# Kernel tuning notes

Measured on AMD Instinct MI355X. Metric: run time of the kernel, lower is better.

## Reference

```python
import jax, jax.numpy as jnp
import numpy as np

B, T, DIM, H = 2, 2048, 1024, 16
HD = DIM // H


def setup_inputs() -> dict:
    key = jax.random.key(0)
    k1, k2, k3 = jax.random.split(key, 3)
    std = 1.0 / np.sqrt(DIM)
    x = jax.random.normal(k1, (B, T, DIM), dtype=jnp.float32)
    # torch Linear(dim, 3*dim).weight is [3*dim, dim]; we store the transposed
    # [dim, 3*dim] layout so forward is x @ W_qkv (same math).
    W_qkv = jax.random.uniform(k2, (DIM, 3 * DIM), dtype=jnp.float32, minval=-std, maxval=std)
    W_proj = jax.random.uniform(k3, (DIM, DIM), dtype=jnp.float32, minval=-std, maxval=std)
    return {"x": x, "W_qkv": W_qkv, "W_proj": W_proj}


def reference(x, W_qkv, W_proj):
    Bv, Tv, C = x.shape
    # qkv projection -> [B, T, 3, H, HD] -> q,k,v each [B, H, T, HD]
    qkv = (x @ W_qkv).reshape(Bv, Tv, 3, H, HD)
    qkv = jnp.transpose(qkv, (2, 0, 3, 1, 4))
    q, k, v = qkv[0], qkv[1], qkv[2]
    scale = jnp.asarray(np.sqrt(HD), dtype=x.dtype)
    scores = jnp.einsum('bhqd,bhkd->bhqk', q, k) / scale
    causal = jnp.tril(jnp.ones((Tv, Tv), dtype=bool))  # [T, T]
    scores = jnp.where(causal[None, None, :, :], scores, -jnp.inf)
    attn = jax.nn.softmax(scores, axis=-1)  # [B, H, T, T]
    # entropy per query position, averaged over heads -> [B, T]
    entropy = -(attn * jnp.log(attn + 1e-9)).sum(axis=-1).mean(axis=1)
    # dropout is identity in eval mode
    out = jnp.einsum('bhqk,bhkd->bhqd', attn, v)
    out = jnp.transpose(out, (0, 2, 1, 3)).reshape(Bv, Tv, C)
    return out @ W_proj, entropy
```

## Files before the change

kernel.cpp:

```cpp
#include <hip/hip_runtime.h>


typedef unsigned short u16;
typedef __attribute__((ext_vector_type(8))) __bf16 bf16x8;
typedef __attribute__((ext_vector_type(4))) float float4v;

#define BQ 2
#define TQ 2048
#define DIMQ 1024
#define HQ 16
#define HDQ 64

__device__ __forceinline__ float4v mfma16(bf16x8 a, bf16x8 b, float4v c) {
    return __builtin_amdgcn_mfma_f32_16x16x32_bf16(a, b, c, 0, 0, 0);
}

__device__ __forceinline__ u16 f2bf(float f) {
    unsigned x = __float_as_uint(f);
    return (u16)((x + 0x7FFFu + ((x >> 16) & 1u)) >> 16);
}

__device__ __forceinline__ uint4 cvt8(float4 a, float4 b) {
    union { uint4 v; u16 u[8]; } r;
    r.u[0] = f2bf(a.x); r.u[1] = f2bf(a.y); r.u[2] = f2bf(a.z); r.u[3] = f2bf(a.w);
    r.u[4] = f2bf(b.x); r.u[5] = f2bf(b.y); r.u[6] = f2bf(b.z); r.u[7] = f2bf(b.w);
    return r.v;
}

__device__ __forceinline__ void async16(const u16* g, u16* l) {
    __builtin_amdgcn_global_load_lds(
        (const __attribute__((address_space(1))) void*)g,
        (__attribute__((address_space(3))) void*)l, 16, 0, 0);
}

__device__ __forceinline__ void tr_tile(
    const float* __restrict__ in, u16* __restrict__ out, int R, int C,
    int tx, int ty, int tid, float (*T)[68])
{
    const int k0 = ty * 64, n0 = tx * 64;
    {
        int r = tid >> 2, cc = (tid & 3) << 4;
        const float* src = in + (size_t)(k0 + r) * C + n0 + cc;
        float4 v0 = ((const float4*)src)[0];
        float4 v1 = ((const float4*)src)[1];
        float4 v2 = ((const float4*)src)[2];
        float4 v3 = ((const float4*)src)[3];
        *(float4*)&T[r][cc + 0]  = v0;
        *(float4*)&T[r][cc + 4]  = v1;
        *(float4*)&T[r][cc + 8]  = v2;
        *(float4*)&T[r][cc + 12] = v3;
    }
    __syncthreads();
    {
        int nr = tid >> 2, kc = (tid & 3) << 4;
        union { uint4 v; u16 u[8]; } o0, o1;
#pragma unroll
        for (int j = 0; j < 8; ++j) o0.u[j] = f2bf(T[kc + j][nr]);
#pragma unroll
        for (int j = 0; j < 8; ++j) o1.u[j] = f2bf(T[kc + 8 + j][nr]);
        u16* dst = out + (size_t)(n0 + nr) * R + k0 + kc;
        ((uint4*)dst)[0] = o0.v;
        *(uint4*)(dst + 8) = o1.v;
    }
}

__global__ __launch_bounds__(256) void prep_kernel(
    const float* __restrict__ x, const float* __restrict__ Wq,
    const float* __restrict__ Wp,
    u16* __restrict__ xb, u16* __restrict__ Wt, u16* __restrict__ Wpt)
{
    __shared__ float T[64][68];
    const int bx = blockIdx.x, tid = threadIdx.x;
    if (bx < 2048) {
        int i = (bx * 256 + tid) * 8;
        float4 a = *(const float4*)(x + i);
        float4 b = *(const float4*)(x + i + 4);
        *(uint4*)(xb + i) = cvt8(a, b);
    } else if (bx < 2816) {
        int bb = bx - 2048;
        tr_tile(Wq, Wt, DIMQ, 3 * DIMQ, bb % 48, bb / 48, tid, T);
    } else {
        int bb = bx - 2816;
        tr_tile(Wp, Wpt, DIMQ, DIMQ, bb & 15, bb >> 4, tid, T);
    }
}

__global__ __launch_bounds__(256) void tr_cvt(
    const float* __restrict__ in, u16* __restrict__ out, int R, int C)
{
    __shared__ float T[64][68];
    tr_tile(in, out, R, C, blockIdx.x, blockIdx.y, threadIdx.x, T);
}

template <int TILEM, int MODE>
__global__ __launch_bounds__(256) void gemm_db(
    const u16* __restrict__ A, const u16* __restrict__ Bt,
    int M, int N, int K,
    u16* __restrict__ Qo, u16* __restrict__ Ko, u16* __restrict__ Vt,
    float* __restrict__ Of, const float* __restrict__ EntIn)
{
    constexpr int MT = TILEM / 32;
    constexpr int AR = TILEM / 64;
    __shared__ u16 As[2][TILEM * 32];
    __shared__ u16 Bs[2][128 * 32];

    const int tid = threadIdx.x;
    const int bm = blockIdx.y, bn = blockIdx.x;
    const int wave = tid >> 6, lane = tid & 63;
    const int quad = lane >> 4, c = lane & 15;
    const int wm = wave >> 1, wn = wave & 1;
    const int x3 = c & 3;

    const float4v z = {0.f, 0.f, 0.f, 0.f};
    float4v acc[MT][4];
#pragma unroll
    for (int mt = 0; mt < MT; ++mt)
#pragma unroll
        for (int tn = 0; tn < 4; ++tn) acc[mt][tn] = z;

    const int srow = tid >> 2;
    const int schunk8 = (((tid & 3) ^ (srow & 3)) << 3);
    const u16* ga = A  + (size_t)(bm * TILEM + srow) * K + schunk8;
    const u16* gb = Bt + (size_t)(bn * 128  + srow) * K + schunk8;

#pragma unroll
    for (int p = 0; p < AR; ++p)
        async16(ga + (size_t)(p * 64) * K, As[0] + p * 2048 + tid * 8);
#pragma unroll
    for (int p = 0; p < 2; ++p)
        async16(gb + (size_t)(p * 64) * K, Bs[0] + p * 2048 + tid * 8);

    const int niter = K >> 5;
    for (int it = 0; it < niter; ++it) {
        __syncthreads();
        if (it + 1 < niter) {
            const int nb = (it + 1) & 1;
            const int kc = (it + 1) * 32;
#pragma unroll
            for (int p = 0; p < AR; ++p)
                async16(ga + kc + (size_t)(p * 64) * K, As[nb] + p * 2048 + tid * 8);
#pragma unroll
            for (int p = 0; p < 2; ++p)
                async16(gb + kc + (size_t)(p * 64) * K, Bs[nb] + p * 2048 + tid * 8);
        }
        const u16* as = As[it & 1];
        const u16* bs = Bs[it & 1];

        bf16x8 af[MT], bfr[4];
#pragma unroll
        for (int mt = 0; mt < MT; ++mt)
            af[mt] = *(const bf16x8*)&as[(wm * (TILEM / 2) + mt * 16 + c) * 32 +
                                         ((quad ^ x3) << 3)];
#pragma unroll
        for (int tn = 0; tn < 4; ++tn)
            bfr[tn] = *(const bf16x8*)&bs[(wn * 64 + tn * 16 + c) * 32 +
                                          ((quad ^ x3) << 3)];
#pragma unroll
        for (int mt = 0; mt < MT; ++mt)
#pragma unroll
            for (int tn = 0; tn < 4; ++tn)
                acc[mt][tn] = mfma16(af[mt], bfr[tn], acc[mt][tn]);
    }

#pragma unroll
    for (int mt = 0; mt < MT; ++mt)
#pragma unroll
        for (int tn = 0; tn < 4; ++tn) {
            int gm0 = bm * TILEM + wm * (TILEM / 2) + mt * 16 + quad * 4;
            int gn  = bn * 128 + wn * 64 + tn * 16 + c;
            if (MODE == 0) {
                int s = gn >> 10, h = (gn >> 6) & 15, d = gn & 63;
                int b = gm0 >> 11, t0 = gm0 & 2047;
                size_t bh = (size_t)(b * HQ + h);
                if (s == 2) {
                    union { unsigned long long w; u16 u[4]; } pk;
#pragma unroll
                    for (int r = 0; r < 4; ++r) pk.u[r] = f2bf(acc[mt][tn][r]);
                    *(unsigned long long*)&Vt[(bh * HDQ + d) * TQ + t0] = pk.w;
                } else {
                    u16* dst = (s == 0) ? Qo : Ko;
                    float sc = (s == 0) ? 0.125f : 1.0f;
#pragma unroll
                    for (int r = 0; r < 4; ++r)
                        dst[(bh * TQ + t0 + r) * HDQ + d] = f2bf(acc[mt][tn][r] * sc);
                }
            } else {
#pragma unroll
                for (int r = 0; r < 4; ++r)
                    Of[(size_t)(gm0 + r) * N + gn] = acc[mt][tn][r];
            }
        }

    if (MODE == 1 && bn == 0 && bm < 16) {
        int i = bm * 256 + tid;
        int b = i >> 11, t = i & 2047;
        float s = 0.f;
#pragma unroll
        for (int h = 0; h < HQ; ++h) s += EntIn[((size_t)(b * HQ + h)) * TQ + t];
        Of[(size_t)BQ * TQ * DIMQ + i] = s * (1.0f / HQ);
    }
}

__global__ __launch_bounds__(256) void attn_kernel(
    const u16* __restrict__ Q, const u16* __restrict__ K,
    const u16* __restrict__ Vt, u16* __restrict__ AO,
    float* __restrict__ Ent)
{
    const int qt1 = blockIdx.x;
    const int qt2 = 31 - qt1;
    const int bh = blockIdx.y;
    const int tid = threadIdx.x;
    const int wave = tid >> 6, lane = tid & 63;
    const int quad = lane >> 4, c = lane & 15;
    const int x7 = c & 7;

    __shared__ u16 Ks[2][64 * 64];
    __shared__ u16 Vs[2][64 * 64];
    __shared__ u16 Ps[4][16 * 64];

    const u16* Qp = Q  + (size_t)bh * TQ * HDQ;
    const u16* Kp = K  + (size_t)bh * TQ * HDQ;
    const u16* Vp = Vt + (size_t)bh * HDQ * TQ;

    const int q0[2] = { qt1 * 64 + wave * 16, qt2 * 64 + wave * 16 };

    bf16x8 qf[2][2];
#pragma unroll
    for (int s = 0; s < 2; ++s) {
        const u16* qr = Qp + (size_t)(q0[s] + c) * HDQ;
        qf[s][0] = *(const bf16x8*)(qr + quad * 8);
        qf[s][1] = *(const bf16x8*)(qr + 32 + quad * 8);
    }

    const float4v z = {0.f, 0.f, 0.f, 0.f};
    float4v oacc[2][4];
#pragma unroll
    for (int s = 0; s < 2; ++s)
#pragma unroll
        for (int tn = 0; tn < 4; ++tn) oacc[s][tn] = z;
    float lp[2] = {0.f, 0.f}, tp[2] = {0.f, 0.f};
    const float MX = 12.0f;

    u16* psw = &Ps[wave][0];
    const int ntile = qt2 + 1;

    const int srow = tid >> 3;
    const int schunk8 = (((tid & 7) ^ (srow & 7)) << 3);
    const u16* ka = Kp + (size_t)srow * HDQ + schunk8;
    const u16* va = Vp + (size_t)srow * TQ + schunk8;

    {
        async16(ka, Ks[0] + tid * 8);
        async16(ka + (size_t)32 * HDQ, Ks[0] + 2048 + tid * 8);
        async16(va, Vs[0] + tid * 8);
        async16(va + (size_t)32 * TQ, Vs[0] + 2048 + tid * 8);
    }

    for (int jt = 0; jt < ntile; ++jt) {
        __syncthreads();
        if (jt + 1 < ntile) {
            int nb = (jt + 1) & 1;
            async16(ka + (size_t)((jt + 1) * 64) * HDQ, Ks[nb] + tid * 8);
            async16(ka + (size_t)((jt + 1) * 64 + 32) * HDQ, Ks[nb] + 2048 + tid * 8);
            async16(va + (jt + 1) * 64, Vs[nb] + tid * 8);
            async16(va + (size_t)32 * TQ + (jt + 1) * 64, Vs[nb] + 2048 + tid * 8);
        }
        const u16* ksb = Ks[jt & 1];
        const u16* vsb = Vs[jt & 1];

        bf16x8 kf[4][2], vf[4][2];
#pragma unroll
        for (int tn = 0; tn < 4; ++tn) {
            int base = (tn * 16 + c) * 64;
            kf[tn][0] = *(const bf16x8*)&ksb[base + ((quad ^ x7) << 3)];
            kf[tn][1] = *(const bf16x8*)&ksb[base + (((quad + 4) ^ x7) << 3)];
            vf[tn][0] = *(const bf16x8*)&vsb[base + ((quad ^ x7) << 3)];
            vf[tn][1] = *(const bf16x8*)&vsb[base + (((quad + 4) ^ x7) << 3)];
        }

#pragma unroll
        for (int s = 0; s < 2; ++s) {
            if (s == 0 && jt > qt1) continue;
            const int diag = s ? qt2 : qt1;
#pragma unroll
            for (int tn = 0; tn < 4; ++tn) {
                float4v sacc = z;
                sacc = mfma16(kf[tn][0], qf[s][0], sacc);
                sacc = mfma16(kf[tn][1], qf[s][1], sacc);
                if (jt == diag) {
#pragma unroll
                    for (int r = 0; r < 4; ++r) {
                        int kg = jt * 64 + tn * 16 + quad * 4 + r;
                        if (kg > q0[s] + c) sacc[r] = -1e30f;
                    }
                }
                unsigned u[4];
#pragma unroll
                for (int r = 0; r < 4; ++r) {
                    float sv = sacc[r];
                    float p = __expf(sv - MX);
                    lp[s] += p;
                    tp[s] += p * sv;
                    u[r] = __float_as_uint(p);
                }
                uint2 pk;
                pk.x = (u[0] >> 16) | (u[1] & 0xffff0000u);
                pk.y = (u[2] >> 16) | (u[3] & 0xffff0000u);
                int kc8 = tn * 2 + (quad >> 1);
                *(uint2*)&psw[c * 64 + ((kc8 ^ x7) << 3) + (quad & 1) * 4] = pk;
            }
            bf16x8 pf0 = *(const bf16x8*)&psw[c * 64 + ((quad ^ x7) << 3)];
            bf16x8 pf1 = *(const bf16x8*)&psw[c * 64 + (((quad + 4) ^ x7) << 3)];
#pragma unroll
            for (int tn = 0; tn < 4; ++tn) {
                oacc[s][tn] = mfma16(vf[tn][0], pf0, oacc[s][tn]);
                oacc[s][tn] = mfma16(vf[tn][1], pf1, oacc[s][tn]);
            }
        }
    }

#pragma unroll
    for (int s = 0; s < 2; ++s) {
        lp[s] += __shfl_xor(lp[s], 16); lp[s] += __shfl_xor(lp[s], 32);
        tp[s] += __shfl_xor(tp[s], 16); tp[s] += __shfl_xor(tp[s], 32);
    }

    const int b = bh >> 4, h = bh & 15;
#pragma unroll
    for (int s = 0; s < 2; ++s) {
        float inv = 1.0f / lp[s];
        u16* dst = AO + ((size_t)(b * TQ + q0[s] + c)) * DIMQ + h * HDQ;
#pragma unroll
        for (int tn = 0; tn < 4; ++tn) {
            unsigned u[4];
#pragma unroll
            for (int r = 0; r < 4; ++r)
                u[r] = (unsigned)f2bf(oacc[s][tn][r] * inv);
            uint2 pk;
            pk.x = u[0] | (u[1] << 16);
            pk.y = u[2] | (u[3] << 16);
            *(uint2*)(dst + tn * 16 + quad * 4) = pk;
        }
        if (quad == 0)
            Ent[(size_t)bh * TQ + q0[s] + c] =
                MX + logf(lp[s]) - tp[s] / lp[s];
    }
}

extern "C" void kernel_launch(void* const* d_in, const int* in_sizes, int n_in,
                              void* d_out, int out_size, void* d_ws, size_t ws_size,
                              hipStream_t stream) {
    const float* x     = (const float*)d_in[0];
    const float* Wqkv  = (const float*)d_in[1];
    const float* Wproj = (const float*)d_in[2];
    float* out = (float*)d_out;

    const size_t NE = (size_t)BQ * HQ * TQ * HDQ;
    const size_t WQN = (size_t)3 * DIMQ * DIMQ;
    const size_t WPN = (size_t)DIMQ * DIMQ;
    u16* Qb  = (u16*)d_ws;
    u16* Kb  = Qb + NE;
    u16* Vtb = Kb + NE;
    u16* xb  = Vtb + NE;
    u16* Wt  = xb + NE;
    u16* AO  = xb;

    const size_t need = (4 * NE + WQN + WPN) * 2 + (size_t)BQ * HQ * TQ * 4;
    const bool room = ws_size >= need;
    u16* Wpt = room ? (Wt + WQN) : Wt;
    float* Ent = room ? (float*)(Wpt + WPN) : (float*)(Wt + WQN);

    prep_kernel<<<dim3(room ? 3072 : 2816), 256, 0, stream>>>(
        x, Wqkv, Wproj, xb, Wt, Wpt);
    gemm_db<128, 0><<<dim3(24, 32), 256, 0, stream>>>(
        xb, Wt, BQ * TQ, 3 * DIMQ, DIMQ, Qb, Kb, Vtb, nullptr, nullptr);
    if (!room)
        tr_cvt<<<dim3(16, 16), 256, 0, stream>>>(Wproj, Wpt, DIMQ, DIMQ);
    attn_kernel<<<dim3(16, BQ * HQ), 256, 0, stream>>>(Qb, Kb, Vtb, AO, Ent);
    gemm_db<64, 1><<<dim3(8, 64), 256, 0, stream>>>(
        AO, Wpt, BQ * TQ, DIMQ, DIMQ, nullptr, nullptr, nullptr, out, Ent);
}
```

Baseline: 179.3 us.

## Split paired causal q-tiles into one tile per block with longest-first ordering

The attention kernel previously paired q-tile i with tile 31-i in one block so every block had equal causal work, giving 512 blocks. Now each block handles a single 64-row q-tile, the launch is 1024 one-dimensional blocks, and blocks are ordered longest tile first, interleaved across heads, to balance load dynamically and raise occupancy. The bf16 packing of probabilities also moves from a truncating bit-shift to the hardware v_cvt_pk_bf16_f32 instruction. In exchange, K/V tiles are no longer shared between two q-tiles in a block, so global-to-LDS traffic grows.

```diff
diff --git a/kernel.cpp b/kernel.cpp
--- a/kernel.cpp
+++ b/kernel.cpp
@@ -206,9 +206,11 @@
     const u16* __restrict__ Vt, u16* __restrict__ AO,
     float* __restrict__ Ent)
 {
-    const int qt1 = blockIdx.x;
-    const int qt2 = 31 - qt1;
-    const int bh = blockIdx.y;
+    const int d = blockIdx.x;
+    const int j = d >> 3;
+    const int bh = (d & 7) * 4 + (j >> 5);
+    const int qt = 31 - (j & 31);
+
     const int tid = threadIdx.x;
     const int wave = tid >> 6, lane = tid & 63;
     const int quad = lane >> 4, c = lane & 15;
@@ -222,27 +224,24 @@
     const u16* Kp = K  + (size_t)bh * TQ * HDQ;
     const u16* Vp = Vt + (size_t)bh * HDQ * TQ;
 
-    const int q0[2] = { qt1 * 64 + wave * 16, qt2 * 64 + wave * 16 };
-
-    bf16x8 qf[2][2];
-#pragma unroll
-    for (int s = 0; s < 2; ++s) {
-        const u16* qr = Qp + (size_t)(q0[s] + c) * HDQ;
-        qf[s][0] = *(const bf16x8*)(qr + quad * 8);
-        qf[s][1] = *(const bf16x8*)(qr + 32 + quad * 8);
+    const int q0 = qt * 64 + wave * 16;
+
+    bf16x8 qf[2];
+    {
+        const u16* qr = Qp + (size_t)(q0 + c) * HDQ;
+        qf[0] = *(const bf16x8*)(qr + quad * 8);
+        qf[1] = *(const bf16x8*)(qr + 32 + quad * 8);
     }
 
     const float4v z = {0.f, 0.f, 0.f, 0.f};
-    float4v oacc[2][4];
-#pragma unroll
-    for (int s = 0; s < 2; ++s)
-#pragma unroll
-        for (int tn = 0; tn < 4; ++tn) oacc[s][tn] = z;
-    float lp[2] = {0.f, 0.f}, tp[2] = {0.f, 0.f};
+    float4v oacc[4];
+#pragma unroll
+    for (int tn = 0; tn < 4; ++tn) oacc[tn] = z;
+    float lp = 0.f, tp = 0.f;
     const float MX = 12.0f;
 
     u16* psw = &Ps[wave][0];
-    const int ntile = qt2 + 1;
+    const int ntile = qt + 1;
 
     const int srow = tid >> 3;
     const int schunk8 = (((tid & 7) ^ (srow & 7)) << 3);
@@ -279,71 +278,64 @@
         }
 
 #pragma unroll
-        for (int s = 0; s < 2; ++s) {
-            if (s == 0 && jt > qt1) continue;
-            const int diag = s ? qt2 : qt1;
-#pragma unroll
-            for (int tn = 0; tn < 4; ++tn) {
-                float4v sacc = z;
-                sacc = mfma16(kf[tn][0], qf[s][0], sacc);
-                sacc = mfma16(kf[tn][1], qf[s][1], sacc);
-                if (jt == diag) {
-#pragma unroll
-                    for (int r = 0; r < 4; ++r) {
-                        int kg = jt * 64 + tn * 16 + quad * 4 + r;
-                        if (kg > q0[s] + c) sacc[r] = -1e30f;
-                    }
+        for (int tn = 0; tn < 4; ++tn) {
+            float4v sacc = z;
+            sacc = mfma16(kf[tn][0], qf[0], sacc);
+            sacc = mfma16(kf[tn][1], qf[1], sacc);
+            if (jt == qt) {
+#pragma unroll
+                for (int r = 0; r < 4; ++r) {
+                    int kg = jt * 64 + tn * 16 + quad * 4 + r;
+                    if (kg > q0 + c) sacc[r] = -1e30f;
                 }
-                unsigned u[4];
-#pragma unroll
-                for (int r = 0; r < 4; ++r) {
-                    float sv = sacc[r];
-                    float p = __expf(sv - MX);
-                    lp[s] += p;
-                    tp[s] += p * sv;
-                    u[r] = __float_as_uint(p);
-                }
-                uint2 pk;
-                pk.x = (u[0] >> 16) | (u[1] & 0xffff0000u);
-                pk.y = (u[2] >> 16) | (u[3] & 0xffff0000u);
-                int kc8 = tn * 2 + (quad >> 1);
-                *(uint2*)&psw[c * 64 + ((kc8 ^ x7) << 3) + (quad & 1) * 4] = pk;
             }
-            bf16x8 pf0 = *(const bf16x8*)&psw[c * 64 + ((quad ^ x7) << 3)];
-            bf16x8 pf1 = *(const bf16x8*)&psw[c * 64 + (((quad + 4) ^ x7) << 3)];
-#pragma unroll
-            for (int tn = 0; tn < 4; ++tn) {
-                oacc[s][tn] = mfma16(vf[tn][0], pf0, oacc[s][tn]);
-                oacc[s][tn] = mfma16(vf[tn][1], pf1, oacc[s][tn]);
+            float pv[4];
+#pragma unroll
+            for (int r = 0; r < 4; ++r) {
+                float sv = sacc[r];
+                float p = __expf(sv - MX);
+                lp += p;
+                tp += p * sv;
+                pv[r] = p;
             }
-        }
-    }
-
-#pragma unroll
-    for (int s = 0; s < 2; ++s) {
-        lp[s] += __shfl_xor(lp[s], 16); lp[s] += __shfl_xor(lp[s], 32);
-        tp[s] += __shfl_xor(tp[s], 16); tp[s] += __shfl_xor(tp[s], 32);
-    }
+            uint2 pk;
+            asm("v_cvt_pk_bf16_f32 %0, %1, %2"
+                : "=v"(pk.x) : "v"(pv[0]), "v"(pv[1]));
+            asm("v_cvt_pk_bf16_f32 %0, %1, %2"
+                : "=v"(pk.y) : "v"(pv[2]), "v"(pv[3]));
+            int kc8 = tn * 2 + (quad >> 1);
+            *(uint2*)&psw[c * 64 + ((kc8 ^ x7) << 3) + (quad & 1) * 4] = pk;
+        }
+        bf16x8 pf0 = *(const bf16x8*)&psw[c * 64 + ((quad ^ x7) << 3)];
+        bf16x8 pf1 = *(const bf16x8*)&psw[c * 64 + (((quad + 4) ^ x7) << 3)];
+#pragma unroll
+        for (int tn = 0; tn < 4; ++tn) {
+            oacc[tn] = mfma16(vf[tn][0], pf0, oacc[tn]);
+            oacc[tn] = mfma16(vf[tn][1], pf1, oacc[tn]);
+        }
+    }
+
+    lp += __shfl_xor(lp, 16); lp += __shfl_xor(lp, 32);
+    tp += __shfl_xor(tp, 16); tp += __shfl_xor(tp, 32);
 
     const int b = bh >> 4, h = bh & 15;
-#pragma unroll
-    for (int s = 0; s < 2; ++s) {
-        float inv = 1.0f / lp[s];
-        u16* dst = AO + ((size_t)(b * TQ + q0[s] + c)) * DIMQ + h * HDQ;
+    {
+        float inv = 1.0f / lp;
+        u16* dst = AO + ((size_t)(b * TQ + q0 + c)) * DIMQ + h * HDQ;
 #pragma unroll
         for (int tn = 0; tn < 4; ++tn) {
             unsigned u[4];
 #pragma unroll
             for (int r = 0; r < 4; ++r)
-                u[r] = (unsigned)f2bf(oacc[s][tn][r] * inv);
+                u[r] = (unsigned)f2bf(oacc[tn][r] * inv);
             uint2 pk;
             pk.x = u[0] | (u[1] << 16);
             pk.y = u[2] | (u[3] << 16);
             *(uint2*)(dst + tn * 16 + quad * 4) = pk;
         }
         if (quad == 0)
-            Ent[(size_t)bh * TQ + q0[s] + c] =
-                MX + logf(lp[s]) - tp[s] / lp[s];
+            Ent[(size_t)bh * TQ + q0 + c] =
+                MX + logf(lp) - tp / lp;
     }
 }
 
@@ -376,7 +368,7 @@
         xb, Wt, BQ * TQ, 3 * DIMQ, DIMQ, Qb, Kb, Vtb, nullptr, nullptr);
     if (!room)
         tr_cvt<<<dim3(16, 16), 256, 0, stream>>>(Wproj, Wpt, DIMQ, DIMQ);
-    attn_kernel<<<dim3(16, BQ * HQ), 256, 0, stream>>>(Qb, Kb, Vtb, AO, Ent);
+    attn_kernel<<<dim3(32 * BQ * HQ), 256, 0, stream>>>(Qb, Kb, Vtb, AO, Ent);
     gemm_db<64, 1><<<dim3(8, 64), 256, 0, stream>>>(
         AO, Wpt, BQ * TQ, DIMQ, DIMQ, nullptr, nullptr, nullptr, out, Ent);
 }
```

Measured after the change: 185.0 us. 3.2% more time.
